# Kernel optimization log

Measured on AMD Instinct MI355X. Metric: run time of the kernel, lower is better.

The kernel has to match this reference:

```python
import jax, jax.numpy as jnp
import numpy as np

LINHAS, COLUNAS, DIM, BATCH = 32, 32, 256, 2048
NEURONS = LINHAS * COLUNAS
TAXA_INICIAL = 0.5
SIGMA_INICIAL = max(LINHAS, COLUNAS) / 2.0  # 16.0


def _grid_locs():
    # matches tf.meshgrid default 'xy' indexing, stacked then flattened
    x = jnp.arange(LINHAS, dtype=jnp.float32)
    y = jnp.arange(COLUNAS, dtype=jnp.float32)
    g = jnp.stack(jnp.meshgrid(x, y), axis=-1)  # (COLUNAS, LINHAS, 2)
    return g.reshape(-1, 2)


def setup_inputs() -> dict:
    key = jax.random.key(0)
    k1, k2 = jax.random.split(key)
    X = jax.random.normal(k1, (BATCH, DIM), dtype=jnp.float32)
    # keras 'random_normal' initializer: stddev 0.05
    pesos = jax.random.normal(k2, (NEURONS, DIM), dtype=jnp.float32) * 0.05
    return {
        "X": X,
        "pesos": pesos,
        "localizacoes": _grid_locs(),
        "passo_atual": 100,
        "total_passos": 1000,
    }


def reference(X, pesos, localizacoes, passo_atual, total_passos):
    frac = jnp.float32(passo_atual) / jnp.float32(total_passos)
    taxa = TAXA_INICIAL * jnp.exp(-frac)
    sigma = SIGMA_INICIAL * jnp.exp(-frac)

    # squared-euclidean distances (B, N)
    x2 = jnp.sum(X * X, axis=1, keepdims=True)
    w2 = jnp.sum(pesos * pesos, axis=1)
    dist = x2 + w2 - 2.0 * (X @ pesos.T)

    bmu_idx = jnp.argmin(dist, axis=1)            # (B,)
    bmu_loc = localizacoes[bmu_idx]               # (B, 2)

    # grid distances and Gaussian neighborhood (B, N)
    dist_grade = jnp.sum((localizacoes[None, :, :] - bmu_loc[:, None, :]) ** 2, axis=2)
    h = jnp.exp(-dist_grade / (2.0 * sigma ** 2))

    # delta_total = mean_b taxa * h[b,n] * (X[b,d] - W[n,d]), computed without
    # materializing the (B, N, D) tensor:
    B = jnp.float32(X.shape[0])
    delta_total = taxa * (jnp.einsum('bn,bd->nd', h, X) - jnp.sum(h, axis=0)[:, None] * pesos) / B

    new_pesos = pesos + delta_total
    return new_pesos
```

## Files before the change

kernel.cpp:

```cpp
#include <hip/hip_runtime.h>
#include <float.h>

#define Bsz 2048
#define Nn  1024
#define Dd  256

typedef __attribute__((ext_vector_type(8))) short bf16x8;
typedef __attribute__((ext_vector_type(4))) float f32x4;
typedef unsigned long long u64;

union b8u4 { bf16x8 v; uint4 u; };

__device__ __forceinline__ void som_params(const int* __restrict__ step,
                                           const int* __restrict__ total,
                                           float* taxa, float* inv2s2) {
    float frac = (float)(*step) / (float)(*total);
    float e = __expf(-frac);
    *taxa = 0.5f * e;
    float sigma = 16.0f * e;
    *inv2s2 = 1.0f / (2.0f * sigma * sigma);
}

__device__ __forceinline__ u64 packsc(float f, int n) {
    unsigned u = __float_as_uint(f);
    u = (u & 0x80000000u) ? ~u : (u | 0x80000000u);
    return ((u64)u << 32) | (unsigned)n;
}

__device__ __forceinline__ float split8t(const float* __restrict__ src,
                                         bf16x8* hi, bf16x8* lo) {
    float4 v0 = *(const float4*)src;
    float4 v1 = *(const float4*)(src + 4);
    float f[8] = {v0.x, v0.y, v0.z, v0.w, v1.x, v1.y, v1.z, v1.w};
    float s = 0.f;
    unsigned hp[4], lp[4];
    #pragma unroll
    for (int p = 0; p < 4; ++p) {
        float a = f[2*p], b = f[2*p+1];
        unsigned ua = __float_as_uint(a), ub = __float_as_uint(b);
        unsigned ha = ua & 0xffff0000u, hb = ub & 0xffff0000u;
        float la = a - __uint_as_float(ha);
        float lb = b - __uint_as_float(hb);
        hp[p] = (ua >> 16) | hb;
        lp[p] = (__float_as_uint(la) >> 16) | (__float_as_uint(lb) & 0xffff0000u);
        s = fmaf(a, a, s); s = fmaf(b, b, s);
    }
    b8u4 H, L;
    H.u = make_uint4(hp[0], hp[1], hp[2], hp[3]);
    L.u = make_uint4(lp[0], lp[1], lp[2], lp[3]);
    *hi = H.v; *lo = L.v;
    return s;
}

__global__ __launch_bounds__(256) void bmu_pre(
    const float* __restrict__ X, const float* __restrict__ W,
    u64* __restrict__ ppack)
{
    __shared__ u64 lmin[2][2][64];

    const int t = threadIdx.x, bid = blockIdx.x;
    const int w = t >> 6, l = t & 63;
    const int lr = l & 15, lg = l >> 4;

    const int wm = w & 1, wn = w >> 1;
    const int b0 = (bid >> 4) * 128 + wm * 64;
    const int n0 = (bid & 15) * 64 + wn * 32;

    f32x4 acc[4][2];
    #pragma unroll
    for (int m = 0; m < 4; ++m)
        #pragma unroll
        for (int n = 0; n < 2; ++n) { f32x4 z = {0.f,0.f,0.f,0.f}; acc[m][n] = z; }
    float w2a[2] = {0.f, 0.f};

    #pragma unroll 2
    for (int kd = 0; kd < Dd; kd += 32) {
        bf16x8 ah[4], al[4], bh[2], bl[2];
        #pragma unroll
        for (int m = 0; m < 4; ++m)
            split8t(&X[(size_t)(b0 + m*16 + lr) * Dd + kd + lg*8], &ah[m], &al[m]);
        #pragma unroll
        for (int nf = 0; nf < 2; ++nf)
            w2a[nf] += split8t(&W[(size_t)(n0 + nf*16 + lr) * Dd + kd + lg*8],
                               &bh[nf], &bl[nf]);
        #pragma unroll
        for (int m = 0; m < 4; ++m)
            #pragma unroll
            for (int nf = 0; nf < 2; ++nf) {
                acc[m][nf] = __builtin_amdgcn_mfma_f32_16x16x32_bf16(ah[m], bh[nf], acc[m][nf], 0, 0, 0);
                acc[m][nf] = __builtin_amdgcn_mfma_f32_16x16x32_bf16(ah[m], bl[nf], acc[m][nf], 0, 0, 0);
                acc[m][nf] = __builtin_amdgcn_mfma_f32_16x16x32_bf16(al[m], bh[nf], acc[m][nf], 0, 0, 0);
            }
    }

    #pragma unroll
    for (int nf = 0; nf < 2; ++nf) {
        w2a[nf] += __shfl_xor(w2a[nf], 16, 64);
        w2a[nf] += __shfl_xor(w2a[nf], 32, 64);
    }
    const int ni0 = n0 + lr, ni1 = n0 + 16 + lr;

    #pragma unroll
    for (int m = 0; m < 4; ++m)
        #pragma unroll
        for (int r = 0; r < 4; ++r) {
            u64 p0 = packsc(w2a[0] - 2.f * acc[m][0][r], ni0);
            u64 p1 = packsc(w2a[1] - 2.f * acc[m][1][r], ni1);
            u64 pm = p1 < p0 ? p1 : p0;
            #pragma unroll
            for (int msk = 1; msk < 16; msk <<= 1) {
                unsigned plo = (unsigned)pm, phi = (unsigned)(pm >> 32);
                plo = __shfl_xor(plo, msk, 64);
                phi = __shfl_xor(phi, msk, 64);
                u64 o = ((u64)phi << 32) | plo;
                if (o < pm) pm = o;
            }
            if (lr == 0) lmin[wm][wn][m*16 + lg*4 + r] = pm;
        }
    __syncthreads();
    if (t < 128) {
        const int bwm = t >> 6, bb = t & 63;
        u64 a = lmin[bwm][0][bb], c = lmin[bwm][1][bb];
        u64 pm = c < a ? c : a;
        const int b = (bid >> 4) * 128 + bwm * 64 + bb;
        ppack[(size_t)(bid & 15) * Bsz + b] = pm;
    }
}

__global__ __launch_bounds__(256) void scatter_t(
    const float* __restrict__ X, const u64* __restrict__ ppack,
    const int* __restrict__ step, const int* __restrict__ total,
    float* __restrict__ T, int* __restrict__ cnt_g)
{
    __shared__ ushort list[Bsz];
    __shared__ float  Ex_l[32][32];
    __shared__ int    psum[256];
    __shared__ int    cnt32[32];

    const int t = threadIdx.x, bid = blockIdx.x;
    const int gy = bid >> 3, dc = bid & 7, d0 = dc * 32;

    float taxa, inv2s2;
    som_params(step, total, &taxa, &inv2s2);

    if (t < 32) cnt32[t] = 0;
    #pragma unroll
    for (int i = 0; i < 4; ++i) {
        int idx = t + 256*i;
        int nx = idx >> 5, gx = idx & 31;
        float d = (float)(nx - gx);
        Ex_l[nx][gx] = __expf(-(d*d) * inv2s2);
    }
    __syncthreads();

    int g8[8];
    int mycnt = 0;
    #pragma unroll
    for (int i = 0; i < 8; ++i) {
        const int b = t + 256*i;
        u64 pm = ppack[b];
        #pragma unroll
        for (int g = 1; g < 16; ++g) {
            u64 c = ppack[(size_t)g * Bsz + b];
            if (c < pm) pm = c;
        }
        g8[i] = (int)(pm & 0xffffu);
        bool m = (g8[i] >> 5) == gy;
        mycnt += m ? 1 : 0;
        if (m && dc == 0) atomicAdd(&cnt32[g8[i] & 31], 1);
    }

    psum[t] = mycnt;
    __syncthreads();
    #pragma unroll
    for (int off = 1; off < 256; off <<= 1) {
        int v = (t >= off) ? psum[t - off] : 0;
        __syncthreads();
        psum[t] += v;
        __syncthreads();
    }
    const int nmatch = psum[255];
    int pos = psum[t] - mycnt;
    #pragma unroll
    for (int i = 0; i < 8; ++i) {
        const int b = t + 256*i;
        if ((g8[i] >> 5) == gy) list[pos++] = (ushort)((b << 5) | (g8[i] & 31));
    }
    if (dc == 0 && t < 32) cnt_g[gy*32 + t] = cnt32[t];
    __syncthreads();

    const int nx = t >> 3, dq = t & 7;
    float4 a = make_float4(0.f, 0.f, 0.f, 0.f);
    for (int k = 0; k < nmatch; ++k) {
        const int rec = list[k];
        const int b = rec >> 5, bx = rec & 31;
        const float ex = Ex_l[nx][bx];
        float4 xv = *(const float4*)&X[(size_t)b * Dd + d0 + dq*4];
        a.x = fmaf(ex, xv.x, a.x);
        a.y = fmaf(ex, xv.y, a.y);
        a.z = fmaf(ex, xv.z, a.z);
        a.w = fmaf(ex, xv.w, a.w);
    }
    *(float4*)&T[(size_t)(gy*32 + nx) * Dd + d0 + dq*4] = a;
}

__global__ __launch_bounds__(256) void finish(
    const float* __restrict__ T, const int* __restrict__ cnt_g,
    const float* __restrict__ W, const int* __restrict__ step,
    const int* __restrict__ total, float* __restrict__ out)
{
    __shared__ float Exc_l[4][32];
    __shared__ float hsum_l[4];

    const int t = threadIdx.x, bid = blockIdx.x;
    const int n0 = bid * 4;
    const int ny = n0 >> 5;
    const int nxb = n0 & 31;

    float taxa, inv2s2;
    som_params(step, total, &taxa, &inv2s2);
    const float invB = 1.0f / 2048.0f;

    if (t < 128) {
        const int nxl = t >> 5, gy = t & 31;
        const int nx = nxb + nxl;
        float s = 0.f;
        #pragma unroll
        for (int gx = 0; gx < 32; ++gx) {
            float d = (float)(nx - gx);
            s = fmaf(__expf(-(d*d) * inv2s2), (float)cnt_g[gy*32 + gx], s);
        }
        Exc_l[nxl][gy] = s;
    }
    __syncthreads();
    if (t < 4) {
        float s = 0.f;
        #pragma unroll
        for (int gy = 0; gy < 32; ++gy) {
            float d = (float)(ny - gy);
            s = fmaf(__expf(-(d*d) * inv2s2), Exc_l[t][gy], s);
        }
        hsum_l[t] = s;
    }
    __syncthreads();

    float ey[32];
    #pragma unroll
    for (int gy = 0; gy < 32; ++gy) {
        float d = (float)(ny - gy);
        ey[gy] = __expf(-(d*d) * inv2s2);
    }

    #pragma unroll
    for (int nl = 0; nl < 4; ++nl) {
        const int n = n0 + nl;
        const int nx = nxb + nl;
        float acc = 0.f;
        #pragma unroll
        for (int gy = 0; gy < 32; ++gy)
            acc = fmaf(ey[gy], T[(size_t)(gy*32 + nx) * Dd + t], acc);
        const float wv = W[(size_t)n * Dd + t];
        out[(size_t)n * Dd + t] = wv + taxa * (acc - hsum_l[nl] * wv) * invB;
    }
}

extern "C" void kernel_launch(void* const* d_in, const int* in_sizes, int n_in,
                              void* d_out, int out_size, void* d_ws, size_t ws_size,
                              hipStream_t stream)
{
    const float* X    = (const float*)d_in[0];
    const float* W    = (const float*)d_in[1];
    const int* step   = (const int*)d_in[3];
    const int* total  = (const int*)d_in[4];
    float* out = (float*)d_out;

    char* p = (char*)d_ws;
    u64*   ppack = (u64*)p;   p += 262144;
    float* T     = (float*)p; p += 1048576;
    int*   cnt   = (int*)p;   p += 4096;

    bmu_pre  <<<256, 256, 0, stream>>>(X, W, ppack);
    scatter_t<<<256, 256, 0, stream>>>(X, ppack, step, total, T, cnt);
    finish   <<<256, 256, 0, stream>>>(T, cnt, W, step, total, out);
}
```

Before: 40.18 us.

## Precompute bf16 hi/lo splits and row norms in a separate prep kernel

```diff
diff --git a/kernel.cpp b/kernel.cpp
--- a/kernel.cpp
+++ b/kernel.cpp
@@ -9,7 +9,14 @@
 typedef __attribute__((ext_vector_type(4))) float f32x4;
 typedef unsigned long long u64;
 
-union b8u4 { bf16x8 v; uint4 u; };
+__device__ __forceinline__ unsigned short bfr(float x) {
+    unsigned u = __float_as_uint(x);
+    u += 0x7fffu + ((u >> 16) & 1u);
+    return (unsigned short)(u >> 16);
+}
+__device__ __forceinline__ float bf2f(unsigned short h) {
+    return __uint_as_float(((unsigned)h) << 16);
+}
 
 __device__ __forceinline__ void som_params(const int* __restrict__ step,
                                            const int* __restrict__ total,
@@ -27,34 +34,46 @@
     return ((u64)u << 32) | (unsigned)n;
 }
 
-__device__ __forceinline__ float split8t(const float* __restrict__ src,
-                                         bf16x8* hi, bf16x8* lo) {
-    float4 v0 = *(const float4*)src;
-    float4 v1 = *(const float4*)(src + 4);
-    float f[8] = {v0.x, v0.y, v0.z, v0.w, v1.x, v1.y, v1.z, v1.w};
-    float s = 0.f;
-    unsigned hp[4], lp[4];
-    #pragma unroll
-    for (int p = 0; p < 4; ++p) {
-        float a = f[2*p], b = f[2*p+1];
-        unsigned ua = __float_as_uint(a), ub = __float_as_uint(b);
-        unsigned ha = ua & 0xffff0000u, hb = ub & 0xffff0000u;
-        float la = a - __uint_as_float(ha);
-        float lb = b - __uint_as_float(hb);
-        hp[p] = (ua >> 16) | hb;
-        lp[p] = (__float_as_uint(la) >> 16) | (__float_as_uint(lb) & 0xffff0000u);
-        s = fmaf(a, a, s); s = fmaf(b, b, s);
-    }
-    b8u4 H, L;
-    H.u = make_uint4(hp[0], hp[1], hp[2], hp[3]);
-    L.u = make_uint4(lp[0], lp[1], lp[2], lp[3]);
-    *hi = H.v; *lo = L.v;
-    return s;
-}
-
-__global__ __launch_bounds__(256) void bmu_pre(
+__global__ __launch_bounds__(256) void prep_split(
     const float* __restrict__ X, const float* __restrict__ W,
-    u64* __restrict__ ppack)
+    ushort* __restrict__ Xhi, ushort* __restrict__ Xlo,
+    ushort* __restrict__ Whi, ushort* __restrict__ Wlo,
+    float* __restrict__ w2)
+{
+    const int t = threadIdx.x, bid = blockIdx.x;
+    const int lane = t & 63;
+
+    if (bid < 256) {
+        int row = bid * 4 + (t >> 6);
+        float4 v = ((const float4*)(W + (size_t)row * Dd))[lane];
+        float s = v.x*v.x + v.y*v.y + v.z*v.z + v.w*v.w;
+        #pragma unroll
+        for (int m = 32; m; m >>= 1) s += __shfl_xor(s, m, 64);
+        if (lane == 0) w2[row] = s;
+        ushort4 h4, l4;
+        h4.x = bfr(v.x); l4.x = bfr(v.x - bf2f(h4.x));
+        h4.y = bfr(v.y); l4.y = bfr(v.y - bf2f(h4.y));
+        h4.z = bfr(v.z); l4.z = bfr(v.z - bf2f(h4.z));
+        h4.w = bfr(v.w); l4.w = bfr(v.w - bf2f(h4.w));
+        *(ushort4*)&Whi[(size_t)row * Dd + lane * 4] = h4;
+        *(ushort4*)&Wlo[(size_t)row * Dd + lane * 4] = l4;
+    } else {
+        int row = (bid - 256) * 4 + (t >> 6);
+        float4 v = ((const float4*)(X + (size_t)row * Dd))[lane];
+        ushort4 h4, l4;
+        h4.x = bfr(v.x); l4.x = bfr(v.x - bf2f(h4.x));
+        h4.y = bfr(v.y); l4.y = bfr(v.y - bf2f(h4.y));
+        h4.z = bfr(v.z); l4.z = bfr(v.z - bf2f(h4.z));
+        h4.w = bfr(v.w); l4.w = bfr(v.w - bf2f(h4.w));
+        *(ushort4*)&Xhi[(size_t)row * Dd + lane * 4] = h4;
+        *(ushort4*)&Xlo[(size_t)row * Dd + lane * 4] = l4;
+    }
+}
+
+__global__ __launch_bounds__(256) void bmu_mfma(
+    const ushort* __restrict__ Xhi, const ushort* __restrict__ Xlo,
+    const ushort* __restrict__ Whi, const ushort* __restrict__ Wlo,
+    const float* __restrict__ w2, u64* __restrict__ ppack)
 {
     __shared__ u64 lmin[2][2][64];
 
@@ -71,18 +90,26 @@
     for (int m = 0; m < 4; ++m)
         #pragma unroll
         for (int n = 0; n < 2; ++n) { f32x4 z = {0.f,0.f,0.f,0.f}; acc[m][n] = z; }
-    float w2a[2] = {0.f, 0.f};
+
+    float w2v[2];
+    #pragma unroll
+    for (int nf = 0; nf < 2; ++nf) w2v[nf] = w2[n0 + nf*16 + lr];
 
     #pragma unroll 2
     for (int kd = 0; kd < Dd; kd += 32) {
         bf16x8 ah[4], al[4], bh[2], bl[2];
         #pragma unroll
-        for (int m = 0; m < 4; ++m)
-            split8t(&X[(size_t)(b0 + m*16 + lr) * Dd + kd + lg*8], &ah[m], &al[m]);
-        #pragma unroll
-        for (int nf = 0; nf < 2; ++nf)
-            w2a[nf] += split8t(&W[(size_t)(n0 + nf*16 + lr) * Dd + kd + lg*8],
-                               &bh[nf], &bl[nf]);
+        for (int m = 0; m < 4; ++m) {
+            size_t off = (size_t)(b0 + m*16 + lr) * Dd + kd + lg*8;
+            ah[m] = *(const bf16x8*)&Xhi[off];
+            al[m] = *(const bf16x8*)&Xlo[off];
+        }
+        #pragma unroll
+        for (int nf = 0; nf < 2; ++nf) {
+            size_t off = (size_t)(n0 + nf*16 + lr) * Dd + kd + lg*8;
+            bh[nf] = *(const bf16x8*)&Whi[off];
+            bl[nf] = *(const bf16x8*)&Wlo[off];
+        }
         #pragma unroll
         for (int m = 0; m < 4; ++m)
             #pragma unroll
@@ -93,19 +120,14 @@
             }
     }
 
-    #pragma unroll
-    for (int nf = 0; nf < 2; ++nf) {
-        w2a[nf] += __shfl_xor(w2a[nf], 16, 64);
-        w2a[nf] += __shfl_xor(w2a[nf], 32, 64);
-    }
     const int ni0 = n0 + lr, ni1 = n0 + 16 + lr;
 
     #pragma unroll
     for (int m = 0; m < 4; ++m)
         #pragma unroll
         for (int r = 0; r < 4; ++r) {
-            u64 p0 = packsc(w2a[0] - 2.f * acc[m][0][r], ni0);
-            u64 p1 = packsc(w2a[1] - 2.f * acc[m][1][r], ni1);
+            u64 p0 = packsc(w2v[0] - 2.f * acc[m][0][r], ni0);
+            u64 p1 = packsc(w2v[1] - 2.f * acc[m][1][r], ni1);
             u64 pm = p1 < p0 ? p1 : p0;
             #pragma unroll
             for (int msk = 1; msk < 16; msk <<= 1) {
@@ -275,11 +297,17 @@
     float* out = (float*)d_out;
 
     char* p = (char*)d_ws;
-    u64*   ppack = (u64*)p;   p += 262144;
-    float* T     = (float*)p; p += 1048576;
-    int*   cnt   = (int*)p;   p += 4096;
-
-    bmu_pre  <<<256, 256, 0, stream>>>(X, W, ppack);
-    scatter_t<<<256, 256, 0, stream>>>(X, ppack, step, total, T, cnt);
-    finish   <<<256, 256, 0, stream>>>(T, cnt, W, step, total, out);
-}
+    u64*   ppack = (u64*)p;    p += 262144;
+    float* T     = (float*)p;  p += 1048576;
+    int*   cnt   = (int*)p;    p += 4096;
+    float* w2    = (float*)p;  p += 4096;
+    ushort* Xhi  = (ushort*)p; p += 1048576;
+    ushort* Xlo  = (ushort*)p; p += 1048576;
+    ushort* Whi  = (ushort*)p; p += 524288;
+    ushort* Wlo  = (ushort*)p; p += 524288;
+
+    prep_split<<<768, 256, 0, stream>>>(X, W, Xhi, Xlo, Whi, Wlo, w2);
+    bmu_mfma  <<<256, 256, 0, stream>>>(Xhi, Xlo, Whi, Wlo, w2, ppack);
+    scatter_t <<<256, 256, 0, stream>>>(X, ppack, step, total, T, cnt);
+    finish    <<<256, 256, 0, stream>>>(T, cnt, W, step, total, out);
+}
```

Result: slower. 45.92 us (+14.3%).
